# Kernel optimization log

Measured on AMD Instinct MI355X. Metric: run time of the kernel, lower is better.

## Reference

```python
import jax, jax.numpy as jnp
import numpy as np

N = 50000
K = 4
D_IN = 256
D_OUT = 64
E = 800000

def setup_inputs() -> dict:
    key = jax.random.key(0)
    k1, k2, k3, k4, k5 = jax.random.split(key, 5)
    x = jax.random.normal(k1, (N, K, D_IN), dtype=jnp.float32)
    weight = jax.random.normal(k2, (D_IN, D_OUT), dtype=jnp.float32) * (1.0 / np.sqrt(D_IN))
    adj_rows = jax.random.randint(k3, (E,), 0, N, dtype=jnp.int32)
    adj_cols = jax.random.randint(k4, (E,), 0, N, dtype=jnp.int32)
    adj_vals = jax.random.uniform(k5, (E,), dtype=jnp.float32)
    return {"x": x, "weight": weight, "adj_rows": adj_rows, "adj_cols": adj_cols, "adj_vals": adj_vals}

def reference(x, weight, adj_rows, adj_cols, adj_vals):
    # x: [N, K, D_in]; weight: [D_in, D_out]
    # dropout p=0.0 / eval mode -> identity
    # support = x @ W for every sample k, vectorized over K
    support = jnp.einsum('nkd,df->nkf', x, weight)          # [N, K, D_out]
    # sparse adj matmul: out[r] += vals[e] * support[cols[e]]
    msgs = adj_vals[:, None, None] * support[adj_cols]       # [E, K, D_out]
    out = jax.ops.segment_sum(msgs, adj_rows, num_segments=N)  # [N, K, D_out]
    return jax.nn.relu(out)
```

## Files before the change

kernel.cpp:

```cpp
#include <hip/hip_runtime.h>
#include <stdint.h>

#define D_IN   256
#define D_OUT  64
#define KHEADS 4
#define ROWLEN 256
#define GBM    128
#define CAP    128

typedef __attribute__((ext_vector_type(8))) short bf16x8;
typedef __attribute__((ext_vector_type(4))) float f32x4;

__device__ __forceinline__ unsigned cvt_pk_bf16(float lo, float hi) {
  unsigned r;
  asm("v_cvt_pk_bf16_f32 %0, %1, %2" : "=v"(r) : "v"(lo), "v"(hi));
  return r;
}

__device__ __forceinline__ bf16x8 pack8(f32x4 a, f32x4 b) {
  union { unsigned u[4]; bf16x8 v; } r;
  r.u[0] = cvt_pk_bf16(a[0], a[1]);
  r.u[1] = cvt_pk_bf16(a[2], a[3]);
  r.u[2] = cvt_pk_bf16(b[0], b[1]);
  r.u[3] = cvt_pk_bf16(b[2], b[3]);
  return r.v;
}

__global__ __launch_bounds__(256) void prep_w(const float* __restrict__ W,
                                              unsigned short* __restrict__ WbT) {
  int idx = blockIdx.x * 256 + threadIdx.x;
  int n  = idx >> 6;
  int k0 = (idx & 63) << 2;
  float w0 = W[(size_t)(k0 + 0) * D_OUT + n];
  float w1 = W[(size_t)(k0 + 1) * D_OUT + n];
  float w2 = W[(size_t)(k0 + 2) * D_OUT + n];
  float w3 = W[(size_t)(k0 + 3) * D_OUT + n];
  unsigned p0 = cvt_pk_bf16(w0, w1);
  unsigned p1 = cvt_pk_bf16(w2, w3);
  *(uint2*)&WbT[(size_t)n * D_IN + k0] = make_uint2(p0, p1);
}

__device__ __forceinline__ void gemm_body(const float* __restrict__ X,
                                          const unsigned short* __restrict__ WbT,
                                          signed char* __restrict__ Sq,
                                          float* __restrict__ scaleArr,
                                          int M, int Nnodes, int g) {
  const int t    = threadIdx.x;
  const int wave = t >> 6;
  const int lane = t & 63;
  const int q    = lane >> 4;
  const int l16  = lane & 15;
  const long row0 = (long)g * GBM;

  long r0 = row0 + wave * 32 + l16;       if (r0 > (long)M - 1) r0 = M - 1;
  long r1 = row0 + wave * 32 + 16 + l16;  if (r1 > (long)M - 1) r1 = M - 1;
  const float* __restrict__ x0 = X + r0 * D_IN + q * 8;
  const float* __restrict__ x1 = X + r1 * D_IN + q * 8;
  const unsigned short* __restrict__ wrow = WbT + (size_t)l16 * D_IN + q * 8;

  f32x4 acc[2][4];
#pragma unroll
  for (int rb = 0; rb < 2; ++rb)
#pragma unroll
    for (int cb = 0; cb < 4; ++cb) acc[rb][cb] = (f32x4){0.f, 0.f, 0.f, 0.f};

  f32x4 c00 = __builtin_nontemporal_load((const f32x4*)(x0));
  f32x4 c01 = __builtin_nontemporal_load((const f32x4*)(x0 + 4));
  f32x4 c10 = __builtin_nontemporal_load((const f32x4*)(x1));
  f32x4 c11 = __builtin_nontemporal_load((const f32x4*)(x1 + 4));
#pragma unroll
  for (int s = 0; s < 8; ++s) {
    f32x4 n00, n01, n10, n11;
    if (s < 7) {
      const float* p0 = x0 + (s + 1) * 32;
      const float* p1 = x1 + (s + 1) * 32;
      n00 = __builtin_nontemporal_load((const f32x4*)(p0));
      n01 = __builtin_nontemporal_load((const f32x4*)(p0 + 4));
      n10 = __builtin_nontemporal_load((const f32x4*)(p1));
      n11 = __builtin_nontemporal_load((const f32x4*)(p1 + 4));
    }
    bf16x8 a0 = pack8(c00, c01);
    bf16x8 a1 = pack8(c10, c11);
#pragma unroll
    for (int cb = 0; cb < 4; ++cb) {
      bf16x8 b = *(const bf16x8*)(wrow + (size_t)cb * 16 * D_IN + s * 32);
      acc[0][cb] = __builtin_amdgcn_mfma_f32_16x16x32_bf16(a0, b, acc[0][cb], 0, 0, 0);
      acc[1][cb] = __builtin_amdgcn_mfma_f32_16x16x32_bf16(a1, b, acc[1][cb], 0, 0, 0);
    }
    if (s < 7) { c00 = n00; c01 = n01; c10 = n10; c11 = n11; }
  }

  float nm0 = 0.f, nm1 = 0.f;
#pragma unroll
  for (int cb = 0; cb < 4; ++cb)
#pragma unroll
    for (int reg = 0; reg < 4; ++reg) {
      nm0 = fmaxf(nm0, fabsf(acc[0][cb][reg]));
      nm1 = fmaxf(nm1, fabsf(acc[1][cb][reg]));
    }
#pragma unroll
  for (int d = 1; d < 16; d <<= 1) {
    nm0 = fmaxf(nm0, __shfl_xor(nm0, d, 64));
    nm1 = fmaxf(nm1, __shfl_xor(nm1, d, 64));
  }
  const float inv0 = (nm0 > 0.f) ? 127.f / nm0 : 0.f;
  const float inv1 = (nm1 > 0.f) ? 127.f / nm1 : 0.f;
  const int node_base = g * 32 + wave * 8;
  if (l16 == 0) {
    int n0 = node_base + q;
    int n1 = node_base + 4 + q;
    if (n0 < Nnodes) scaleArr[n0] = nm0 / 127.f;
    if (n1 < Nnodes) scaleArr[n1] = nm1 / 127.f;
  }
#pragma unroll
  for (int rb = 0; rb < 2; ++rb) {
    const float inv = rb ? inv1 : inv0;
#pragma unroll
    for (int cb = 0; cb < 4; ++cb)
#pragma unroll
      for (int reg = 0; reg < 4; ++reg) {
        long r = row0 + wave * 32 + rb * 16 + q * 4 + reg;
        if (r < M) {
          int qi = (int)rintf(acc[rb][cb][reg] * inv);
          Sq[r * D_OUT + cb * 16 + l16] = (signed char)qi;
        }
      }
  }
}

__device__ __forceinline__ void place_body(const int* __restrict__ rows,
                                           const int* __restrict__ cols,
                                           const float* __restrict__ vals,
                                           int* __restrict__ cnt,
                                           uint2* __restrict__ ecv, int E, int pb) {
  int e = pb * 256 + threadIdx.x;
  if (e < E) {
    int r = rows[e];
    int c = cols[e];
    float v = vals[e];
    int pos = atomicAdd(&cnt[r], 1);
    if (pos < CAP)
      ecv[((size_t)r << 7) + pos] = make_uint2((unsigned)c, __float_as_uint(v));
  }
}

__global__ __launch_bounds__(256) void fused_phase1(
    const float* __restrict__ X, const unsigned short* __restrict__ WbT,
    signed char* __restrict__ Sq, float* __restrict__ scaleArr,
    const int* __restrict__ rows, const int* __restrict__ cols,
    const float* __restrict__ vals, int* __restrict__ cnt,
    uint2* __restrict__ ecv, int M, int Nnodes, int E, int G, int P) {
  const int bid = blockIdx.x;
  const int g = bid / 3, r3 = bid - 3 * g;
  if (r3 == 0) {
    if (g < G) gemm_body(X, WbT, Sq, scaleArr, M, Nnodes, g);
  } else {
    int pb = 2 * g + r3 - 1;
    if (pb < P) place_body(rows, cols, vals, cnt, ecv, E, pb);
  }
}

__global__ __launch_bounds__(256) void gather_kernel(
    const int* __restrict__ Sqi, const float* __restrict__ scaleArr,
    const int* __restrict__ cnt, const uint2* __restrict__ ecv,
    float* __restrict__ out, int n) {
  const int lane = threadIdx.x & 63;
  const int r = blockIdx.x * 4 + (threadIdx.x >> 6);
  if (r >= n) return;
  int deg = cnt[r];
  if (deg > CAP) deg = CAP;
  const uint2* __restrict__ bucket = ecv + ((size_t)r << 7);

  unsigned long long bl =
      __builtin_nontemporal_load((const unsigned long long*)bucket + lane);
  const unsigned mc = (lane < deg) ? (unsigned)bl : 0u;
  const float    mv = (lane < deg)
      ? __uint_as_float((unsigned)(bl >> 32)) * scaleArr[mc] : 0.f;

  float4 a0 = make_float4(0.f, 0.f, 0.f, 0.f);
  float4 a1 = a0, a2 = a0, a3 = a0;
  const int d0  = deg < 64 ? deg : 64;
  const int nd0 = (d0 + 7) & ~7;
  for (int i = 0; i < nd0; i += 8) {
    unsigned cc[8]; float vv[8]; int ww[8];
#pragma unroll
    for (int u = 0; u < 8; ++u) {
      cc[u] = __shfl(mc, i + u);
      vv[u] = __shfl(mv, i + u);
    }
#pragma unroll
    for (int u = 0; u < 8; ++u) ww[u] = Sqi[(size_t)cc[u] * 64 + lane];
#pragma unroll
    for (int u = 0; u < 8; ++u) {
      float4& a = ((u & 3) == 0) ? a0 : (((u & 3) == 1) ? a1 : (((u & 3) == 2) ? a2 : a3));
      const float v = vv[u];
      const int   w = ww[u];
      a.x += v * (float)(w << 24 >> 24);
      a.y += v * (float)(w << 16 >> 24);
      a.z += v * (float)(w <<  8 >> 24);
      a.w += v * (float)(w >> 24);
    }
  }
  if (deg > 64) {
    unsigned long long bl1 = *((const unsigned long long*)bucket + 64 + lane);
    const unsigned mc1 = (64 + lane < deg) ? (unsigned)bl1 : 0u;
    const float    mv1 = (64 + lane < deg)
        ? __uint_as_float((unsigned)(bl1 >> 32)) * scaleArr[mc1] : 0.f;
    const int ndt = ((deg - 64) + 7) & ~7;
    for (int i = 0; i < ndt; ++i) {
      const unsigned c = __shfl(mc1, i);
      const float    v = __shfl(mv1, i);
      const int w = Sqi[(size_t)c * 64 + lane];
      a0.x += v * (float)(w << 24 >> 24); a0.y += v * (float)(w << 16 >> 24);
      a0.z += v * (float)(w <<  8 >> 24); a0.w += v * (float)(w >> 24);
    }
  }
  f32x4 res;
  res[0] = fmaxf(a0.x + a1.x + a2.x + a3.x, 0.f);
  res[1] = fmaxf(a0.y + a1.y + a2.y + a3.y, 0.f);
  res[2] = fmaxf(a0.z + a1.z + a2.z + a3.z, 0.f);
  res[3] = fmaxf(a0.w + a1.w + a2.w + a3.w, 0.f);
  __builtin_nontemporal_store(res, (f32x4*)&out[(size_t)r * ROWLEN + (lane << 2)]);
}

extern "C" void kernel_launch(void* const* d_in, const int* in_sizes, int n_in,
                              void* d_out, int out_size, void* d_ws, size_t ws_size,
                              hipStream_t stream) {
  const float* x    = (const float*)d_in[0];
  const float* w    = (const float*)d_in[1];
  const int*   rows = (const int*)d_in[2];
  const int*   cols = (const int*)d_in[3];
  const float* vals = (const float*)d_in[4];
  float* out = (float*)d_out;

  const int E = in_sizes[2];
  const int N = in_sizes[0] / (KHEADS * D_IN);
  const int M = N * KHEADS;

  char* ws = (char*)d_ws;
  size_t o = 0;
  signed char* Sq = (signed char*)(ws + o); o += (size_t)M * D_OUT;
  o = (o + 15) & ~(size_t)15;
  float* scaleArr = (float*)(ws + o); o += (size_t)N * sizeof(float);
  o = (o + 15) & ~(size_t)15;
  int* cnt = (int*)(ws + o); o += (size_t)N * sizeof(int);
  o = (o + 63) & ~(size_t)63;
  unsigned short* WbT = (unsigned short*)(ws + o);
  o += (size_t)D_OUT * D_IN * sizeof(unsigned short);
  o = (o + 15) & ~(size_t)15;
  uint2* ecv = (uint2*)(ws + o);

  (void)hipMemsetAsync(cnt, 0, (size_t)N * sizeof(int), stream);

  const int G = (M + GBM - 1) / GBM;
  const int P = (E + 255) / 256;
  prep_w<<<16, 256, 0, stream>>>(w, WbT);
  fused_phase1<<<3 * G, 256, 0, stream>>>(x, WbT, Sq, scaleArr, rows, cols,
                                          vals, cnt, ecv, M, N, E, G, P);
  gather_kernel<<<(N + 3) / 4, 256, 0, stream>>>((const int*)Sq, scaleArr,
                                                 cnt, ecv, out, N);
}
```

Before: 390.1 us.

## Stage bf16 weights in LDS with padded stride and double block size

The GEMM blocks now copy the transposed bf16 weight matrix into shared memory, using a padded row stride so MFMA B-fragment reads avoid bank conflicts, instead of reading it from global memory every step. Blocks grow to 512 threads (256 GEMM rows per block, 4 placement blocks per GEMM block), and the X loads switch from nontemporal to regular loads. This is meant to cut global/L2 weight traffic and per-block overhead. In exchange it adds an LDS fill plus a barrier per GEMM block, and the 33KB shared allocation also applies to placement blocks, which can limit occupancy.

Result: no change. 389.4 us (-0.2%).

```diff
diff --git a/kernel.cpp b/kernel.cpp
--- a/kernel.cpp
+++ b/kernel.cpp
@@ -5,7 +5,9 @@
 #define D_OUT  64
 #define KHEADS 4
 #define ROWLEN 256
-#define GBM    128
+#define GBM    256
+#define LDW    264
+#define WBT_B  (64 * LDW * 2)
 #define CAP    128
 
 typedef __attribute__((ext_vector_type(8))) short bf16x8;
@@ -17,12 +19,12 @@
   return r;
 }
 
-__device__ __forceinline__ bf16x8 pack8(f32x4 a, f32x4 b) {
+__device__ __forceinline__ bf16x8 pack8(float4 a, float4 b) {
   union { unsigned u[4]; bf16x8 v; } r;
-  r.u[0] = cvt_pk_bf16(a[0], a[1]);
-  r.u[1] = cvt_pk_bf16(a[2], a[3]);
-  r.u[2] = cvt_pk_bf16(b[0], b[1]);
-  r.u[3] = cvt_pk_bf16(b[2], b[3]);
+  r.u[0] = cvt_pk_bf16(a.x, a.y);
+  r.u[1] = cvt_pk_bf16(a.z, a.w);
+  r.u[2] = cvt_pk_bf16(b.x, b.y);
+  r.u[3] = cvt_pk_bf16(b.z, b.w);
   return r.v;
 }
 
@@ -37,14 +39,15 @@
   float w3 = W[(size_t)(k0 + 3) * D_OUT + n];
   unsigned p0 = cvt_pk_bf16(w0, w1);
   unsigned p1 = cvt_pk_bf16(w2, w3);
-  *(uint2*)&WbT[(size_t)n * D_IN + k0] = make_uint2(p0, p1);
+  *(uint2*)&WbT[(size_t)n * LDW + k0] = make_uint2(p0, p1);
 }
 
 __device__ __forceinline__ void gemm_body(const float* __restrict__ X,
                                           const unsigned short* __restrict__ WbT,
                                           signed char* __restrict__ Sq,
                                           float* __restrict__ scaleArr,
-                                          int M, int Nnodes, int g) {
+                                          int M, int Nnodes, int g,
+                                          unsigned short* lWt) {
   const int t    = threadIdx.x;
   const int wave = t >> 6;
   const int lane = t & 63;
@@ -52,11 +55,21 @@
   const int l16  = lane & 15;
   const long row0 = (long)g * GBM;
 
+  {
+    const uint4* __restrict__ src = (const uint4*)WbT;
+    uint4* dst = (uint4*)lWt;
+#pragma unroll
+    for (int r2 = 0; r2 < 5; ++r2) {
+      int slot = t + r2 * 512;
+      if (slot < WBT_B / 16) dst[slot] = src[slot];
+    }
+  }
+  __syncthreads();
+
   long r0 = row0 + wave * 32 + l16;       if (r0 > (long)M - 1) r0 = M - 1;
   long r1 = row0 + wave * 32 + 16 + l16;  if (r1 > (long)M - 1) r1 = M - 1;
   const float* __restrict__ x0 = X + r0 * D_IN + q * 8;
   const float* __restrict__ x1 = X + r1 * D_IN + q * 8;
-  const unsigned short* __restrict__ wrow = WbT + (size_t)l16 * D_IN + q * 8;
 
   f32x4 acc[2][4];
 #pragma unroll
@@ -64,26 +77,25 @@
 #pragma unroll
     for (int cb = 0; cb < 4; ++cb) acc[rb][cb] = (f32x4){0.f, 0.f, 0.f, 0.f};
 
-  f32x4 c00 = __builtin_nontemporal_load((const f32x4*)(x0));
-  f32x4 c01 = __builtin_nontemporal_load((const f32x4*)(x0 + 4));
-  f32x4 c10 = __builtin_nontemporal_load((const f32x4*)(x1));
-  f32x4 c11 = __builtin_nontemporal_load((const f32x4*)(x1 + 4));
+  float4 c00 = *(const float4*)(x0);
+  float4 c01 = *(const float4*)(x0 + 4);
+  float4 c10 = *(const float4*)(x1);
+  float4 c11 = *(const float4*)(x1 + 4);
 #pragma unroll
   for (int s = 0; s < 8; ++s) {
-    f32x4 n00, n01, n10, n11;
+    float4 n00, n01, n10, n11;
     if (s < 7) {
       const float* p0 = x0 + (s + 1) * 32;
       const float* p1 = x1 + (s + 1) * 32;
-      n00 = __builtin_nontemporal_load((const f32x4*)(p0));
-      n01 = __builtin_nontemporal_load((const f32x4*)(p0 + 4));
-      n10 = __builtin_nontemporal_load((const f32x4*)(p1));
-      n11 = __builtin_nontemporal_load((const f32x4*)(p1 + 4));
+      n00 = *(const float4*)(p0); n01 = *(const float4*)(p0 + 4);
+      n10 = *(const float4*)(p1); n11 = *(const float4*)(p1 + 4);
     }
     bf16x8 a0 = pack8(c00, c01);
     bf16x8 a1 = pack8(c10, c11);
+    const unsigned short* wb = &lWt[l16 * LDW + s * 32 + q * 8];
 #pragma unroll
     for (int cb = 0; cb < 4; ++cb) {
-      bf16x8 b = *(const bf16x8*)(wrow + (size_t)cb * 16 * D_IN + s * 32);
+      bf16x8 b = *(const bf16x8*)(wb + cb * 16 * LDW);
       acc[0][cb] = __builtin_amdgcn_mfma_f32_16x16x32_bf16(a0, b, acc[0][cb], 0, 0, 0);
       acc[1][cb] = __builtin_amdgcn_mfma_f32_16x16x32_bf16(a1, b, acc[1][cb], 0, 0, 0);
     }
@@ -105,7 +117,7 @@
   }
   const float inv0 = (nm0 > 0.f) ? 127.f / nm0 : 0.f;
   const float inv1 = (nm1 > 0.f) ? 127.f / nm1 : 0.f;
-  const int node_base = g * 32 + wave * 8;
+  const int node_base = g * 64 + wave * 8;
   if (l16 == 0) {
     int n0 = node_base + q;
     int n1 = node_base + 4 + q;
@@ -133,7 +145,7 @@
                                            const float* __restrict__ vals,
                                            int* __restrict__ cnt,
                                            uint2* __restrict__ ecv, int E, int pb) {
-  int e = pb * 256 + threadIdx.x;
+  int e = pb * 512 + threadIdx.x;
   if (e < E) {
     int r = rows[e];
     int c = cols[e];
@@ -144,18 +156,19 @@
   }
 }
 
-__global__ __launch_bounds__(256) void fused_phase1(
+__global__ __launch_bounds__(512, 8) void fused_phase1(
     const float* __restrict__ X, const unsigned short* __restrict__ WbT,
     signed char* __restrict__ Sq, float* __restrict__ scaleArr,
     const int* __restrict__ rows, const int* __restrict__ cols,
     const float* __restrict__ vals, int* __restrict__ cnt,
     uint2* __restrict__ ecv, int M, int Nnodes, int E, int G, int P) {
+  __shared__ __align__(16) unsigned short lWt[64 * LDW];
   const int bid = blockIdx.x;
-  const int g = bid / 3, r3 = bid - 3 * g;
-  if (r3 == 0) {
-    if (g < G) gemm_body(X, WbT, Sq, scaleArr, M, Nnodes, g);
+  const int g = bid / 5, r5 = bid - 5 * g;
+  if (r5 == 0) {
+    if (g < G) gemm_body(X, WbT, Sq, scaleArr, M, Nnodes, g, lWt);
   } else {
-    int pb = 2 * g + r3 - 1;
+    int pb = 4 * g + r5 - 1;
     if (pb < P) place_body(rows, cols, vals, cnt, ecv, E, pb);
   }
 }
@@ -245,17 +258,16 @@
   o = (o + 15) & ~(size_t)15;
   int* cnt = (int*)(ws + o); o += (size_t)N * sizeof(int);
   o = (o + 63) & ~(size_t)63;
-  unsigned short* WbT = (unsigned short*)(ws + o);
-  o += (size_t)D_OUT * D_IN * sizeof(unsigned short);
+  unsigned short* WbT = (unsigned short*)(ws + o); o += WBT_B;
   o = (o + 15) & ~(size_t)15;
   uint2* ecv = (uint2*)(ws + o);
 
   (void)hipMemsetAsync(cnt, 0, (size_t)N * sizeof(int), stream);
 
   const int G = (M + GBM - 1) / GBM;
-  const int P = (E + 255) / 256;
+  const int P = (E + 511) / 512;
   prep_w<<<16, 256, 0, stream>>>(w, WbT);
-  fused_phase1<<<3 * G, 256, 0, stream>>>(x, WbT, Sq, scaleArr, rows, cols,
+  fused_phase1<<<5 * G, 512, 0, stream>>>(x, WbT, Sq, scaleArr, rows, cols,
                                           vals, cnt, ecv, M, N, E, G, P);
   gather_kernel<<<(N + 3) / 4, 256, 0, stream>>>((const int*)Sq, scaleArr,
                                                  cnt, ecv, out, N);
```
